# Kernel optimization log

Measured on AMD Instinct MI355X. Metric: run time of the kernel, lower is better.

## Reference

```python
import jax, jax.numpy as jnp
import numpy as np
from jax import lax

N_SECTIONS, N_CHANNELS = 8, 128
KT, KF = 32, 16                 # kernel (time, freq)
LPOST = 400                     # section_length_postsyn
LPRE = KT + LPOST - 1           # 431, section_length_presyn
SECTION_DISTANCE = 400          # LPRE - overlap (overlap = 31)
N_TIMESTEPS, FREQ = 3231, 256
THRESHOLD = 15.0


def setup_inputs() -> dict:
    key = jax.random.key(0)
    k1, k2 = jax.random.split(key)
    # scale so mean conv response ~ threshold (512 taps * 0.8 * mean(X))
    X = jax.random.uniform(k1, (N_TIMESTEPS, FREQ), dtype=jnp.float32) * 0.073
    # SpykeTorch Convolution init: N(0.8, 0.05)
    W = 0.8 + 0.05 * jax.random.normal(k2, (N_SECTIONS, N_CHANNELS, 1, KT, KF), dtype=jnp.float32)
    return {"X": X, "W": W}


def _sections(X):
    # [S, LPRE, FREQ] overlapping time windows
    starts = jnp.arange(N_SECTIONS) * SECTION_DISTANCE
    idx = starts[:, None] + jnp.arange(LPRE)
    return X[idx]


def _conv_sections(X, W):
    Xs = _sections(X)  # [S, LPRE, FREQ]
    def conv1(xs, w):
        # xs: [LPRE, FREQ], w: [C, 1, KT, KF] -> [C, LPOST, FOUT]
        return lax.conv_general_dilated(xs[None, None], w, (1, 1), 'VALID')[0]
    return jax.vmap(conv1)(Xs, W)  # [S, C, LPOST, FOUT]


def reference(X, W):
    pots = _conv_sections(X, W)                              # [S, C, 400, 241]
    # sf.fire: zero potentials < threshold, then sign -> binary spikes
    spikes = (pots >= THRESHOLD).astype(pots.dtype)
    # Pooling((LPOST, KF)): max-pool, stride = window, no padding
    pool = lax.reduce_window(spikes, -jnp.inf, lax.max,
                             (1, 1, LPOST, KF), (1, 1, LPOST, KF), 'VALID')  # [S, C, 1, 15]
    # sf.get_k_winners(pool): dim 0 (sections) acts as the time dimension
    T = pool.shape[0]
    spk = jnp.sign(pool)
    earliest = jnp.clip((T - spk.sum(axis=0)).astype(jnp.int32), 0, T - 1)   # [C,1,Fp]
    values = jnp.take_along_axis(pool, earliest[None], axis=0)[0]            # earliest spike value
    trunc = spk * values[None]
    v = trunc.max() * T
    trunc = trunc + spk * v
    total = trunc.sum(axis=0)                                # [C, 1, Fp]
    max_val = total.max()
    # winners[0][0] = feature (channel) index of the flat argmax
    feat = jnp.argmax(total.reshape(-1)) // (total.shape[1] * total.shape[2])
    return jnp.where(max_val != 0, feat, -1).astype(jnp.int32)
```

## Files before the change

kernel.cpp:

```cpp
#include <hip/hip_runtime.h>


using int4v  = __attribute__((ext_vector_type(4))) int;
using int8v  = __attribute__((ext_vector_type(8))) int;
using f32x16 = __attribute__((ext_vector_type(16))) float;

#define THRESH 15.0f
#define SCALE_ONE 0x7F7F7F7F
#define SCALE_Q   0x7D7D7D7D

__device__ __forceinline__ unsigned f4enc(float v) {
  float r2 = __builtin_rintf(v + v);
  float r1 = __builtin_rintf(v);
  return (v <= 2.f) ? (unsigned)r2
       : (v <= 4.f) ? (unsigned)r1 + 2u
       : (v < 5.f)  ? 6u : 7u;
}

__global__ __launch_bounds__(256) void prep_kernel(const float* __restrict__ W,
                                                   unsigned char* __restrict__ Wp4,
                                                   int* __restrict__ pool) {
  int t = blockIdx.x * 256 + threadIdx.x;
  if (t < 15360) pool[t] = 0;
  int s = t >> 11, r = t & 2047, c = r >> 4, b = r & 15;
  const float* src = W + ((s * 128 + c) * 512 + b * 32);
  int4v o;
#pragma unroll
  for (int i = 0; i < 4; ++i) {
    unsigned d = 0;
#pragma unroll
    for (int e = 0; e < 8; ++e)
      d |= f4enc(fmaxf(src[i * 8 + e], 0.f) * 4.f) << (4 * e);
    o[i] = (int)d;
  }
  *(int4v*)(Wp4 + s * 32768 + (b >> 1) * 4096 + (b & 1) * 2048 + c * 16) = o;
}

__global__ __launch_bounds__(256, 2) void conv_pool_kernel(const float* __restrict__ X,
                                                           const unsigned char* __restrict__ Wp4,
                                                           int* __restrict__ pool) {
  __shared__ __align__(16) unsigned char Ash[8 * 1008];
  __shared__ __align__(16) unsigned char Bsh[32768];
  __shared__ unsigned poolbits[32];

  const int tid = threadIdx.x;
  const int bid = blockIdx.x;
  const int s   = bid / 390;
  const int rem = bid % 390;
  const int tt  = rem / 30;
  const int ft  = rem % 30;
  const int t0  = (tt == 12) ? 368 : tt * 32;
  const int fo0 = ft * 8, fp = ft >> 1;
  const int srow = s * 400 + t0;

  if (tid < 32) poolbits[tid] = 0;

  {
    const unsigned char* wbase = Wp4 + s * 32768;
#pragma unroll
    for (int it = 0; it < 8; ++it) {
      int off = (it * 256 + tid) * 16;
      __builtin_amdgcn_global_load_lds(
          (const __attribute__((address_space(1))) void*)(wbase + off),
          (__attribute__((address_space(3))) void*)(&Bsh[off]), 16, 0, 0);
    }
  }

  for (int i = tid; i < 504; i += 256) {
    int d = i / 63, r = i % 63;
    const float* xs = X + (srow + r) * 256 + fo0 + d;
    int4v pk;
#pragma unroll
    for (int h = 0; h < 4; ++h) {
      int q = 0;
      q = __builtin_amdgcn_cvt_pk_fp8_f32(xs[h * 4 + 0], xs[h * 4 + 1], q, false);
      q = __builtin_amdgcn_cvt_pk_fp8_f32(xs[h * 4 + 2], xs[h * 4 + 3], q, true);
      pk[h] = q;
    }
    *(int4v*)&Ash[d * 1008 + r * 16] = pk;
  }

  f32x16 acc[2][4];
#pragma unroll
  for (int a = 0; a < 2; ++a)
#pragma unroll
    for (int b = 0; b < 4; ++b)
#pragma unroll
      for (int e = 0; e < 16; ++e) acc[a][b][e] = 0.f;

  const int w = tid >> 6, l = tid & 63;
  const int m31 = l & 31, ko = l >> 5;

  const int aoff0 = (2 * w) * 1008 + m31 * 16 + ko * 32;
  const int aoff1 = (2 * w + 1) * 1008 + m31 * 16 + ko * 32;
  const int boff  = ko * 2048 + m31 * 16;

  __syncthreads();

#define LOAD_CHUNK(chh, A0v, A1v, Bv)                                          \
  {                                                                            \
    int4v _a0lo = *(const int4v*)&Ash[aoff0 + (chh) * 64];                     \
    int4v _a0hi = *(const int4v*)&Ash[aoff0 + (chh) * 64 + 16];                \
    int4v _a1lo = *(const int4v*)&Ash[aoff1 + (chh) * 64];                     \
    int4v _a1hi = *(const int4v*)&Ash[aoff1 + (chh) * 64 + 16];                \
    A0v = (int8v){_a0lo[0], _a0lo[1], _a0lo[2], _a0lo[3],                      \
                  _a0hi[0], _a0hi[1], _a0hi[2], _a0hi[3]};                     \
    A1v = (int8v){_a1lo[0], _a1lo[1], _a1lo[2], _a1lo[3],                      \
                  _a1hi[0], _a1hi[1], _a1hi[2], _a1hi[3]};                     \
    const unsigned char* _bb = Bsh + (chh) * 4096 + boff;                      \
    Bv[0] = *(const int4v*)(_bb);                                              \
    Bv[1] = *(const int4v*)(_bb + 512);                                        \
    Bv[2] = *(const int4v*)(_bb + 1024);                                       \
    Bv[3] = *(const int4v*)(_bb + 1536);                                       \
  }

#define MFMA_CHUNK(A0v, A1v, Bv)                                               \
  {                                                                            \
    _Pragma("unroll")                                                          \
    for (int nt = 0; nt < 4; ++nt) {                                           \
      int8v Bf = {Bv[nt][0], Bv[nt][1], Bv[nt][2], Bv[nt][3], 0, 0, 0, 0};     \
      acc[0][nt] = __builtin_amdgcn_mfma_scale_f32_32x32x64_f8f6f4(            \
          A0v, Bf, acc[0][nt], 0, 4, 0, SCALE_ONE, 0, SCALE_Q);                \
      acc[1][nt] = __builtin_amdgcn_mfma_scale_f32_32x32x64_f8f6f4(            \
          A1v, Bf, acc[1][nt], 0, 4, 0, SCALE_ONE, 0, SCALE_Q);                \
    }                                                                          \
  }

  {
    int8v A0a, A1a, A0b, A1b;
    int4v Ba[4], Bb[4];
    LOAD_CHUNK(0, A0a, A1a, Ba);
#pragma unroll 1
    for (int ch = 0; ch < 8; ch += 2) {
      LOAD_CHUNK(ch + 1, A0b, A1b, Bb);
      MFMA_CHUNK(A0a, A1a, Ba);
      int chn = (ch + 2 < 8) ? ch + 2 : 7;
      LOAD_CHUNK(chn, A0a, A1a, Ba);
      MFMA_CHUNK(A0b, A1b, Bb);
    }
  }

  unsigned sp = 0;
#pragma unroll
  for (int nt = 0; nt < 4; ++nt) {
    float m0 = -1e30f, m1 = -1e30f;
#pragma unroll
    for (int e = 0; e < 16; ++e) {
      m0 = fmaxf(m0, acc[0][nt][e]);
      m1 = fmaxf(m1, acc[1][nt][e]);
    }
    if (fmaxf(m0, m1) >= THRESH) sp |= (1u << nt);
  }
  sp |= __shfl_xor(sp, 32, 64);
  if (l < 32 && sp) atomicOr(&poolbits[m31], sp);
  __syncthreads();

  if (tid < 128) {
    unsigned bits = poolbits[tid & 31];
    if ((bits >> (tid >> 5)) & 1)
      pool[(s * 128 + tid) * 15 + fp] = 1;
  }
}

__global__ __launch_bounds__(256) void winner_kernel(const int* __restrict__ pool,
                                                     float* __restrict__ out) {
  __shared__ int lp[15360];
  __shared__ int sh_v;
  __shared__ int sh_best;
  int tid = threadIdx.x;
  if (tid == 0) { sh_v = 0; sh_best = 0; }
  for (int i = tid; i < 15360; i += 256) lp[i] = pool[i];
  __syncthreads();

  int localv = 0;
  for (int p = tid; p < 1920; p += 256) {
    int c = p / 15, f = p % 15;
    int cnt = 0;
    for (int s = 0; s < 8; ++s) cnt += lp[(s * 128 + c) * 15 + f];
    if (cnt > 0) {
      int early = 8 - cnt; if (early > 7) early = 7;
      localv |= lp[(early * 128 + c) * 15 + f];
    }
  }
  if (localv) atomicOr(&sh_v, 1);
  __syncthreads();

  const int v = sh_v * 8;
  int localbest = 0;
  for (int p = tid; p < 1920; p += 256) {
    int c = p / 15, f = p % 15;
    int cnt = 0;
    for (int s = 0; s < 8; ++s) cnt += lp[(s * 128 + c) * 15 + f];
    int early = 8 - cnt; if (early > 7) early = 7;
    int val = lp[(early * 128 + c) * 15 + f];
    int total = cnt * (val + v);
    int pack = (total << 12) | (4095 - p);
    if (pack > localbest) localbest = pack;
  }
  atomicMax(&sh_best, localbest);
  __syncthreads();

  if (tid == 0) {
    int total = sh_best >> 12;
    int p = 4095 - (sh_best & 4095);
    int feat = p / 15;
    out[0] = (total != 0) ? (float)feat : -1.0f;
  }
}

extern "C" void kernel_launch(void* const* d_in, const int* in_sizes, int n_in,
                              void* d_out, int out_size, void* d_ws, size_t ws_size,
                              hipStream_t stream) {
  (void)in_sizes; (void)n_in; (void)out_size; (void)ws_size;
  const float* X = (const float*)d_in[0];
  const float* W = (const float*)d_in[1];
  unsigned char* Wp4 = (unsigned char*)d_ws;
  int* pool = (int*)((char*)d_ws + (1 << 18));

  prep_kernel<<<64, 256, 0, stream>>>(W, Wp4, pool);
  conv_pool_kernel<<<3120, 256, 0, stream>>>(X, Wp4, pool);
  winner_kernel<<<1, 256, 0, stream>>>(pool, (float*)d_out);
}
```

Before: 98.74 us.

## Merge two freq tiles per block, staging X once in LDS and reusing B weights

Each block now handles 16 output frequencies (a full pool column) instead of 8, which halves the grid. The 32-column X strip is loaded once into LDS as raw floats, and both 8-wide sub-tiles are converted to fp8 from there. The weight tile B loaded into LDS is reused for both sub-tiles. This removes redundant X global reads and duplicate 32KB weight loads per pool column. In exchange it adds LDS use (about 8KB raw plus 16KB A) and serialises the two sub-tile MFMA passes inside a block, which may reduce occupancy and parallelism.

```diff
diff --git a/kernel.cpp b/kernel.cpp
--- a/kernel.cpp
+++ b/kernel.cpp
@@ -39,18 +39,19 @@
 __global__ __launch_bounds__(256, 2) void conv_pool_kernel(const float* __restrict__ X,
                                                            const unsigned char* __restrict__ Wp4,
                                                            int* __restrict__ pool) {
-  __shared__ __align__(16) unsigned char Ash[8 * 1008];
+  __shared__ __align__(16) float Xraw[63 * 33];
+  __shared__ __align__(16) unsigned char Ash[2 * 8064];
   __shared__ __align__(16) unsigned char Bsh[32768];
   __shared__ unsigned poolbits[32];
 
   const int tid = threadIdx.x;
   const int bid = blockIdx.x;
-  const int s   = bid / 390;
-  const int rem = bid % 390;
-  const int tt  = rem / 30;
-  const int ft  = rem % 30;
+  const int s   = bid / 195;
+  const int rem = bid % 195;
+  const int tt  = rem / 15;
+  const int j   = rem % 15;
   const int t0  = (tt == 12) ? 368 : tt * 32;
-  const int fo0 = ft * 8, fp = ft >> 1;
+  const int fo0 = j * 16;
   const int srow = s * 400 + t0;
 
   if (tid < 32) poolbits[tid] = 0;
@@ -67,17 +68,10 @@
   }
 
   for (int i = tid; i < 504; i += 256) {
-    int d = i / 63, r = i % 63;
-    const float* xs = X + (srow + r) * 256 + fo0 + d;
-    int4v pk;
-#pragma unroll
-    for (int h = 0; h < 4; ++h) {
-      int q = 0;
-      q = __builtin_amdgcn_cvt_pk_fp8_f32(xs[h * 4 + 0], xs[h * 4 + 1], q, false);
-      q = __builtin_amdgcn_cvt_pk_fp8_f32(xs[h * 4 + 2], xs[h * 4 + 3], q, true);
-      pk[h] = q;
-    }
-    *(int4v*)&Ash[d * 1008 + r * 16] = pk;
+    int r = i >> 3, q = i & 7;
+    float4 v = *(const float4*)(X + (srow + r) * 256 + fo0 + q * 4);
+    float* dst = &Xraw[r * 33 + q * 4];
+    dst[0] = v.x; dst[1] = v.y; dst[2] = v.z; dst[3] = v.w;
   }
 
   f32x16 acc[2][4];
@@ -97,12 +91,27 @@
 
   __syncthreads();
 
-#define LOAD_CHUNK(chh, A0v, A1v, Bv)                                          \
-  {                                                                            \
-    int4v _a0lo = *(const int4v*)&Ash[aoff0 + (chh) * 64];                     \
-    int4v _a0hi = *(const int4v*)&Ash[aoff0 + (chh) * 64 + 16];                \
-    int4v _a1lo = *(const int4v*)&Ash[aoff1 + (chh) * 64];                     \
-    int4v _a1hi = *(const int4v*)&Ash[aoff1 + (chh) * 64 + 16];                \
+#define STAGE_TILE(ABASE, cb)                                                  \
+  for (int i = tid; i < 504; i += 256) {                                       \
+    int d = i / 63, r = i % 63;                                                \
+    const float* xr = &Xraw[r * 33 + d + (cb)];                                \
+    int4v pk;                                                                  \
+    _Pragma("unroll")                                                          \
+    for (int h = 0; h < 4; ++h) {                                              \
+      int q = 0;                                                               \
+      q = __builtin_amdgcn_cvt_pk_fp8_f32(xr[h * 4 + 0], xr[h * 4 + 1], q, false); \
+      q = __builtin_amdgcn_cvt_pk_fp8_f32(xr[h * 4 + 2], xr[h * 4 + 3], q, true);  \
+      pk[h] = q;                                                               \
+    }                                                                          \
+    *(int4v*)&Ash[(ABASE) + d * 1008 + r * 16] = pk;                           \
+  }
+
+#define LOAD_CHUNK(ABASE, chh, A0v, A1v, Bv)                                   \
+  {                                                                            \
+    int4v _a0lo = *(const int4v*)&Ash[(ABASE) + aoff0 + (chh) * 64];           \
+    int4v _a0hi = *(const int4v*)&Ash[(ABASE) + aoff0 + (chh) * 64 + 16];      \
+    int4v _a1lo = *(const int4v*)&Ash[(ABASE) + aoff1 + (chh) * 64];           \
+    int4v _a1hi = *(const int4v*)&Ash[(ABASE) + aoff1 + (chh) * 64 + 16];      \
     A0v = (int8v){_a0lo[0], _a0lo[1], _a0lo[2], _a0lo[3],                      \
                   _a0hi[0], _a0hi[1], _a0hi[2], _a0hi[3]};                     \
     A1v = (int8v){_a1lo[0], _a1lo[1], _a1lo[2], _a1lo[3],                      \
@@ -126,31 +135,55 @@
     }                                                                          \
   }
 
-  {
-    int8v A0a, A1a, A0b, A1b;
-    int4v Ba[4], Bb[4];
-    LOAD_CHUNK(0, A0a, A1a, Ba);
-#pragma unroll 1
-    for (int ch = 0; ch < 8; ch += 2) {
-      LOAD_CHUNK(ch + 1, A0b, A1b, Bb);
-      MFMA_CHUNK(A0a, A1a, Ba);
-      int chn = (ch + 2 < 8) ? ch + 2 : 7;
-      LOAD_CHUNK(chn, A0a, A1a, Ba);
-      MFMA_CHUNK(A0b, A1b, Bb);
-    }
-  }
-
-  unsigned sp = 0;
-#pragma unroll
-  for (int nt = 0; nt < 4; ++nt) {
-    float m0 = -1e30f, m1 = -1e30f;
-#pragma unroll
-    for (int e = 0; e < 16; ++e) {
-      m0 = fmaxf(m0, acc[0][nt][e]);
-      m1 = fmaxf(m1, acc[1][nt][e]);
-    }
-    if (fmaxf(m0, m1) >= THRESH) sp |= (1u << nt);
-  }
+#define KLOOP(ABASE)                                                           \
+  {                                                                            \
+    int8v A0a, A1a, A0b, A1b;                                                  \
+    int4v Ba[4], Bb[4];                                                        \
+    LOAD_CHUNK(ABASE, 0, A0a, A1a, Ba);                                        \
+    _Pragma("unroll 1")                                                        \
+    for (int ch = 0; ch < 8; ch += 2) {                                        \
+      LOAD_CHUNK(ABASE, ch + 1, A0b, A1b, Bb);                                 \
+      MFMA_CHUNK(A0a, A1a, Ba);                                                \
+      int chn = (ch + 2 < 8) ? ch + 2 : 7;                                     \
+      LOAD_CHUNK(ABASE, chn, A0a, A1a, Ba);                                    \
+      MFMA_CHUNK(A0b, A1b, Bb);                                                \
+    }                                                                          \
+  }
+
+#define EXTRACT_SP(spv)                                                        \
+  {                                                                            \
+    spv = 0;                                                                   \
+    _Pragma("unroll")                                                          \
+    for (int nt = 0; nt < 4; ++nt) {                                           \
+      float m0 = -1e30f, m1 = -1e30f;                                          \
+      _Pragma("unroll")                                                        \
+      for (int e = 0; e < 16; ++e) {                                           \
+        m0 = fmaxf(m0, acc[0][nt][e]);                                         \
+        m1 = fmaxf(m1, acc[1][nt][e]);                                         \
+      }                                                                        \
+      if (fmaxf(m0, m1) >= THRESH) spv |= (1u << nt);                          \
+    }                                                                          \
+  }
+
+  STAGE_TILE(0, 0)
+  __syncthreads();
+  KLOOP(0)
+  unsigned spA;
+  EXTRACT_SP(spA)
+
+#pragma unroll
+  for (int a = 0; a < 2; ++a)
+#pragma unroll
+    for (int b = 0; b < 4; ++b)
+#pragma unroll
+      for (int e = 0; e < 16; ++e) acc[a][b][e] = 0.f;
+  STAGE_TILE(8064, 8)
+  __syncthreads();
+  KLOOP(8064)
+  unsigned spB;
+  EXTRACT_SP(spB)
+
+  unsigned sp = spA | spB;
   sp |= __shfl_xor(sp, 32, 64);
   if (l < 32 && sp) atomicOr(&poolbits[m31], sp);
   __syncthreads();
@@ -158,7 +191,7 @@
   if (tid < 128) {
     unsigned bits = poolbits[tid & 31];
     if ((bits >> (tid >> 5)) & 1)
-      pool[(s * 128 + tid) * 15 + fp] = 1;
+      pool[(s * 128 + tid) * 15 + j] = 1;
   }
 }
 
@@ -218,6 +251,6 @@
   int* pool = (int*)((char*)d_ws + (1 << 18));
 
   prep_kernel<<<64, 256, 0, stream>>>(W, Wp4, pool);
-  conv_pool_kernel<<<3120, 256, 0, stream>>>(X, Wp4, pool);
+  conv_pool_kernel<<<1560, 256, 0, stream>>>(X, Wp4, pool);
   winner_kernel<<<1, 256, 0, stream>>>(pool, (float*)d_out);
 }
```

New measurement: 114.3 us. +15.7%, slower.
